# Kernel optimization log

Measured on AMD Instinct MI355X. Metric: run time of the kernel, lower is better.

Reference implementation:

```python
import jax, jax.numpy as jnp
import numpy as np

B, T, L, H, D = 1024, 128, 16, 512, 64

def setup_inputs() -> dict:
    key = jax.random.key(0)
    ks = jax.random.split(key, 12)
    s = 0.05  # param init scale to keep gates in a sane range
    return {
        "labels": jax.random.normal(ks[0], (B, L), jnp.float32),
        "z": jax.random.normal(ks[1], (T, B, H), jnp.float32),
        "W1": s * jax.random.normal(ks[2], (H, L), jnp.float32),
        "b1": jnp.zeros((H,), jnp.float32),
        "W2": s * jax.random.normal(ks[3], (H, H), jnp.float32),
        "b2": jnp.zeros((H,), jnp.float32),
        "W3": s * jax.random.normal(ks[4], (H, H), jnp.float32),
        "Wih": s * jax.random.normal(ks[5], (4 * H, H), jnp.float32),
        "Whh": s * jax.random.normal(ks[6], (4 * H, H), jnp.float32),
        "bih": jnp.zeros((4 * H,), jnp.float32),
        "bhh": jnp.zeros((4 * H,), jnp.float32),
        "P1": s * jax.random.normal(ks[7], (H, H), jnp.float32),
        "pb1": jnp.zeros((H,), jnp.float32),
        "P2": s * jax.random.normal(ks[8], (H, H), jnp.float32),
        "pb2": jnp.zeros((H,), jnp.float32),
        "P3": s * jax.random.normal(ks[9], (D, H), jnp.float32),
        "pb3": jnp.zeros((D,), jnp.float32),
    }

def reference(labels, z, W1, b1, W2, b2, W3, Wih, Whh, bih, bhh,
              P1, pb1, P2, pb2, P3, pb3):
    # label_linear MLP: Linear-ReLU-Linear-ReLU-Linear(no bias)
    x = jax.nn.relu(labels @ W1.T + b1)
    x = jax.nn.relu(x @ W2.T + b2)
    conds = x @ W3.T                      # [B, H]

    def step(carry, zt):
        h, c = carry
        inp = conds + zt                  # noise injected each timestep
        gates = inp @ Wih.T + bih + h @ Whh.T + bhh   # [B, 4H]
        i, f, g, o = jnp.split(gates, 4, axis=-1)     # torch LSTMCell gate order
        i = jax.nn.sigmoid(i)
        f = jax.nn.sigmoid(f)
        g = jnp.tanh(g)
        o = jax.nn.sigmoid(o)
        c = f * c + i * g
        h = o * jnp.tanh(c)
        # proj MLP per step
        y = jax.nn.relu(h @ P1.T + pb1)
        y = jax.nn.relu(y @ P2.T + pb2)
        y = y @ P3.T + pb3                # [B, D]
        return (h, c), y

    h0 = jnp.zeros_like(conds)
    c0 = jnp.zeros_like(conds)
    _, ys = jax.lax.scan(step, (h0, c0), z)  # ys: [T, B, D]
    return jnp.transpose(ys, (1, 0, 2))      # [B, T, D] == torch.stack(dim=1)
```

## Files before the change

### kernel.cpp

```cpp
#include <hip/hip_runtime.h>
#include <cstdint>
#include <cstddef>

namespace {

constexpr int Bb = 1024;
constexpr int Tt = 128;
constexpr int Ll = 16;
constexpr int Hh = 512;
constexpr int Dd = 64;
constexpr int Gg = 2048;
constexpr int CH = 16;

typedef _Float16 half8 __attribute__((ext_vector_type(8)));
typedef float f32x4 __attribute__((ext_vector_type(4)));

__device__ __forceinline__ float sigm(float x) { return 1.f / (1.f + __expf(-x)); }
__device__ __forceinline__ float tanh_f(float x) { return 2.f / (1.f + __expf(-2.f * x)) - 1.f; }

__device__ __forceinline__ void gload16(const void* g, void* l) {
  __builtin_amdgcn_global_load_lds(
      (const __attribute__((address_space(1))) void*)g,
      (__attribute__((address_space(3))) void*)l, 16, 0, 0);
}

__global__ void k_wcat(const float* __restrict__ Wih, const float* __restrict__ Whh,
                       _Float16* __restrict__ Wcat) {
  int idx = blockIdx.x * 256 + threadIdx.x;
  int n = idx >> 10, k = idx & 1023;
  float v = (k < Hh) ? Wih[n * Hh + k] : Whh[n * Hh + (k - Hh)];
  Wcat[idx] = (_Float16)v;
}

__global__ void k_cvt(const float* __restrict__ src, _Float16* __restrict__ dst, int n) {
  int idx = blockIdx.x * 256 + threadIdx.x;
  if (idx < n) dst[idx] = (_Float16)src[idx];
}

__global__ void k_gbias(const float* __restrict__ a, const float* __restrict__ b,
                        float* __restrict__ o) {
  int i = blockIdx.x * 256 + threadIdx.x;
  if (i < Gg) o[i] = a[i] + b[i];
}

__global__ void k_label1(const float* __restrict__ labels, const float* __restrict__ W1,
                         const float* __restrict__ b1, _Float16* __restrict__ x1) {
  int idx = blockIdx.x * 256 + threadIdx.x;
  int b = idx >> 9, n = idx & 511;
  const float* lab = labels + b * Ll;
  const float* w = W1 + n * Ll;
  float s = b1[n];
#pragma unroll
  for (int l = 0; l < Ll; ++l) s += lab[l] * w[l];
  x1[idx] = (_Float16)fmaxf(s, 0.f);
}

__global__ void k_init(float* __restrict__ c, _Float16* __restrict__ A0,
                       const float* __restrict__ conds, const float* __restrict__ z0) {
  int idx = blockIdx.x * 256 + threadIdx.x;
  int b = idx >> 9, h = idx & 511;
  c[idx] = 0.f;
  A0[(size_t)b * 1024 + 512 + h] = (_Float16)0.f;
  A0[(size_t)b * 1024 + h] = (_Float16)(conds[idx] + z0[idx]);
}

template <int BM, int BN>
__global__ __launch_bounds__(256) void gemm_tn(
    const _Float16* __restrict__ A, int lda,
    const _Float16* __restrict__ W, int ldb,
    const float* __restrict__ bias,
    float* __restrict__ Cf, _Float16* __restrict__ Ch, int ldc,
    int K, int relu, int out_mode, int t0) {
  constexpr int BK = 64;
  __shared__ __align__(16) _Float16 lA[BM * BK];
  __shared__ __align__(16) _Float16 lB[BN * BK];
  constexpr int WM = BM / 2, WN = BN / 2;
  constexpr int MF = WM / 16, NF = WN / 16;
  const int tid = threadIdx.x;
  const int lane = tid & 63;
  const int wid = tid >> 6;
  const int wm = wid >> 1, wn = wid & 1;
  const long bm0 = (long)blockIdx.x * BM, bn0 = (long)blockIdx.y * BN;
  const int srow = tid >> 3, schunk = tid & 7;

  f32x4 zero4 = {0.f, 0.f, 0.f, 0.f};
  f32x4 acc[MF][NF];
#pragma unroll
  for (int i = 0; i < MF; ++i)
#pragma unroll
    for (int j = 0; j < NF; ++j) acc[i][j] = zero4;

  for (int k0 = 0; k0 < K; k0 += BK) {
#pragma unroll
    for (int i = 0; i < BM / 32; ++i) {
      int row = i * 32 + srow;
      int gc = schunk ^ (row & 7);
      gload16(A + (bm0 + row) * lda + k0 + gc * 8, &lA[row * BK + schunk * 8]);
    }
#pragma unroll
    for (int i = 0; i < BN / 32; ++i) {
      int row = i * 32 + srow;
      int gc = schunk ^ (row & 7);
      gload16(W + (bn0 + row) * ldb + k0 + gc * 8, &lB[row * BK + schunk * 8]);
    }
    __syncthreads();
#pragma unroll
    for (int kk = 0; kk < BK; kk += 32) {
      half8 af[MF], bf[NF];
#pragma unroll
      for (int mi = 0; mi < MF; ++mi) {
        int r = wm * WM + mi * 16 + (lane & 15);
        int c = (kk >> 3) + (lane >> 4);
        af[mi] = *(const half8*)&lA[r * BK + ((c ^ (r & 7)) << 3)];
      }
#pragma unroll
      for (int ni = 0; ni < NF; ++ni) {
        int r = wn * WN + ni * 16 + (lane & 15);
        int c = (kk >> 3) + (lane >> 4);
        bf[ni] = *(const half8*)&lB[r * BK + ((c ^ (r & 7)) << 3)];
      }
#pragma unroll
      for (int mi = 0; mi < MF; ++mi)
#pragma unroll
        for (int ni = 0; ni < NF; ++ni)
          acc[mi][ni] = __builtin_amdgcn_mfma_f32_16x16x32_f16(af[mi], bf[ni], acc[mi][ni], 0, 0, 0);
    }
    __syncthreads();
  }

#pragma unroll
  for (int mi = 0; mi < MF; ++mi) {
#pragma unroll
    for (int ni = 0; ni < NF; ++ni) {
      long col = bn0 + wn * WN + ni * 16 + (lane & 15);
      float bv = bias ? bias[col] : 0.f;
#pragma unroll
      for (int j = 0; j < 4; ++j) {
        long grow = bm0 + wm * WM + mi * 16 + (lane >> 4) * 4 + j;
        float v = acc[mi][ni][j] + bv;
        if (relu) v = fmaxf(v, 0.f);
        if (Ch) {
          Ch[grow * ldc + col] = (_Float16)v;
        } else {
          long off = out_mode ? (((grow & 1023) * Tt + t0 + (grow >> 10)) * Dd + col)
                              : (grow * ldc + col);
          Cf[off] = v;
        }
      }
    }
  }
}

__global__ __launch_bounds__(256) void step_fused(
    const _Float16* __restrict__ Acur,
    const _Float16* __restrict__ Wcat,
    const float* __restrict__ gbias,
    float* __restrict__ c,
    _Float16* __restrict__ Anext,
    _Float16* __restrict__ hchunk,
    const float* __restrict__ conds,
    const float* __restrict__ znext,
    int tloc) {
  constexpr int BK = 64;
  __shared__ __align__(16) _Float16 lA[64 * BK];
  __shared__ __align__(16) _Float16 lB[64 * BK];
  const int tid = threadIdx.x;
  const int lane = tid & 63;
  const int w = tid >> 6;
  const long bm0 = (long)blockIdx.x * 64;
  const int hc0 = blockIdx.y * 16;
  const int srow = tid >> 3, schunk = tid & 7;

  f32x4 zero4 = {0.f, 0.f, 0.f, 0.f};
  f32x4 acc[4];
#pragma unroll
  for (int i = 0; i < 4; ++i) acc[i] = zero4;

  for (int k0 = 0; k0 < 1024; k0 += BK) {
#pragma unroll
    for (int i = 0; i < 2; ++i) {
      int row = i * 32 + srow;
      int gc = schunk ^ (row & 7);
      gload16(Acur + (bm0 + row) * 1024 + k0 + gc * 8, &lA[row * BK + schunk * 8]);
    }
#pragma unroll
    for (int i = 0; i < 2; ++i) {
      int rb = i * 32 + srow;
      long grow = ((long)(rb >> 4) << 9) + hc0 + (rb & 15);
      int gc = schunk ^ (rb & 7);
      gload16(Wcat + grow * 1024 + k0 + gc * 8, &lB[rb * BK + schunk * 8]);
    }
    __syncthreads();
#pragma unroll
    for (int kk = 0; kk < BK; kk += 32) {
      int cch = (kk >> 3) + (lane >> 4);
      int ra = w * 16 + (lane & 15);
      half8 af = *(const half8*)&lA[ra * BK + (((cch ^ (ra & 7))) << 3)];
#pragma unroll
      for (int ni = 0; ni < 4; ++ni) {
        int rb = ni * 16 + (lane & 15);
        half8 bf = *(const half8*)&lB[rb * BK + (((cch ^ (rb & 7))) << 3)];
        acc[ni] = __builtin_amdgcn_mfma_f32_16x16x32_f16(af, bf, acc[ni], 0, 0, 0);
      }
    }
    __syncthreads();
  }

  const int h = hc0 + (lane & 15);
  const float bi = gbias[h];
  const float bf_ = gbias[h + 512];
  const float bg = gbias[h + 1024];
  const float bo = gbias[h + 1536];
#pragma unroll
  for (int j = 0; j < 4; ++j) {
    long b = bm0 + w * 16 + (lane >> 4) * 4 + j;
    long idx = b * 512 + h;
    float iv = sigm(acc[0][j] + bi);
    float fv = sigm(acc[1][j] + bf_);
    float gv = tanh_f(acc[2][j] + bg);
    float ov = sigm(acc[3][j] + bo);
    float cc = fv * c[idx] + iv * gv;
    c[idx] = cc;
    float hh = ov * tanh_f(cc);
    _Float16 hf = (_Float16)hh;
    Anext[b * 1024 + 512 + h] = hf;
    hchunk[(long)tloc * (Bb * Hh) + idx] = hf;
    if (znext) Anext[b * 1024 + h] = (_Float16)(conds[idx] + znext[idx]);
  }
}

}

extern "C" void kernel_launch(void* const* d_in, const int* in_sizes, int n_in,
                              void* d_out, int out_size, void* d_ws, size_t ws_size,
                              hipStream_t stream) {
  const float* labels = (const float*)d_in[0];
  const float* z      = (const float*)d_in[1];
  const float* W1     = (const float*)d_in[2];
  const float* b1     = (const float*)d_in[3];
  const float* W2     = (const float*)d_in[4];
  const float* b2     = (const float*)d_in[5];
  const float* W3     = (const float*)d_in[6];
  const float* Wih    = (const float*)d_in[7];
  const float* Whh    = (const float*)d_in[8];
  const float* bih    = (const float*)d_in[9];
  const float* bhh    = (const float*)d_in[10];
  const float* P1     = (const float*)d_in[11];
  const float* pb1    = (const float*)d_in[12];
  const float* P2     = (const float*)d_in[13];
  const float* pb2    = (const float*)d_in[14];
  const float* P3     = (const float*)d_in[15];
  const float* pb3    = (const float*)d_in[16];
  float* out = (float*)d_out;
  (void)in_sizes; (void)n_in; (void)out_size; (void)ws_size;

  char* p = (char*)d_ws;
  auto alloc = [&](size_t bytes) -> char* {
    char* r = p;
    p += (bytes + 255) & ~(size_t)255;
    return r;
  };
  _Float16* Wcat  = (_Float16*)alloc((size_t)Gg * 1024 * 2);
  _Float16* P1h   = (_Float16*)alloc((size_t)Hh * Hh * 2);
  _Float16* P2h   = (_Float16*)alloc((size_t)Hh * Hh * 2);
  _Float16* P3h   = (_Float16*)alloc((size_t)Dd * Hh * 2);
  _Float16* W2h   = (_Float16*)alloc((size_t)Hh * Hh * 2);
  _Float16* W3h   = (_Float16*)alloc((size_t)Hh * Hh * 2);
  float*    gb    = (float*)alloc((size_t)Gg * 4);
  _Float16* x1    = (_Float16*)alloc((size_t)Bb * Hh * 2);
  _Float16* x2    = (_Float16*)alloc((size_t)Bb * Hh * 2);
  float*    conds = (float*)alloc((size_t)Bb * Hh * 4);
  float*    cbuf  = (float*)alloc((size_t)Bb * Hh * 4);
  _Float16* A0    = (_Float16*)alloc((size_t)Bb * 1024 * 2);
  _Float16* A1    = (_Float16*)alloc((size_t)Bb * 1024 * 2);
  _Float16* hch   = (_Float16*)alloc((size_t)CH * Bb * Hh * 2);
  _Float16* Y1    = (_Float16*)alloc((size_t)CH * Bb * Hh * 2);
  _Float16* Y2    = (_Float16*)alloc((size_t)CH * Bb * Hh * 2);

  dim3 blk(256);

  k_wcat<<<(Gg * 1024) / 256, blk, 0, stream>>>(Wih, Whh, Wcat);
  k_cvt<<<(Hh * Hh) / 256, blk, 0, stream>>>(P1, P1h, Hh * Hh);
  k_cvt<<<(Hh * Hh) / 256, blk, 0, stream>>>(P2, P2h, Hh * Hh);
  k_cvt<<<(Dd * Hh) / 256, blk, 0, stream>>>(P3, P3h, Dd * Hh);
  k_cvt<<<(Hh * Hh) / 256, blk, 0, stream>>>(W2, W2h, Hh * Hh);
  k_cvt<<<(Hh * Hh) / 256, blk, 0, stream>>>(W3, W3h, Hh * Hh);
  k_gbias<<<Gg / 256, blk, 0, stream>>>(bih, bhh, gb);

  k_label1<<<(Bb * Hh) / 256, blk, 0, stream>>>(labels, W1, b1, x1);
  gemm_tn<64, 64><<<dim3(Bb / 64, Hh / 64), blk, 0, stream>>>(
      x1, Hh, W2h, Hh, b2, nullptr, x2, Hh, Hh, 1, 0, 0);
  gemm_tn<64, 64><<<dim3(Bb / 64, Hh / 64), blk, 0, stream>>>(
      x2, Hh, W3h, Hh, nullptr, conds, nullptr, Hh, Hh, 0, 0, 0);

  k_init<<<(Bb * Hh) / 256, blk, 0, stream>>>(cbuf, A0, conds, z);

  for (int t = 0; t < Tt; ++t) {
    const _Float16* Acur = (t & 1) ? A1 : A0;
    _Float16* Anext = (t & 1) ? A0 : A1;
    const float* znext = (t + 1 < Tt) ? (z + (size_t)(t + 1) * Bb * Hh) : nullptr;
    step_fused<<<dim3(Bb / 64, Hh / 16), blk, 0, stream>>>(
        Acur, Wcat, gb, cbuf, Anext, hch, conds, znext, t & (CH - 1));
    if ((t & (CH - 1)) == (CH - 1)) {
      int t0 = t - (CH - 1);
      gemm_tn<128, 128><<<dim3(CH * Bb / 128, Hh / 128), blk, 0, stream>>>(
          hch, Hh, P1h, Hh, pb1, nullptr, Y1, Hh, Hh, 1, 0, 0);
      gemm_tn<128, 128><<<dim3(CH * Bb / 128, Hh / 128), blk, 0, stream>>>(
          Y1, Hh, P2h, Hh, pb2, nullptr, Y2, Hh, Hh, 1, 0, 0);
      gemm_tn<64, 64><<<dim3(CH * Bb / 64, Dd / 64), blk, 0, stream>>>(
          Y2, Hh, P3h, Hh, pb3, out, nullptr, Dd, Hh, 0, 1, t0);
    }
  }
}
```

Before: 2.769 ms.

## Double-buffer LDS in GEMMs, remap step blocks per XCD, enlarge chunk size

Adds double-buffered LDS staging to the generic GEMM and the fused LSTM step so the next K tile loads while MFMAs run on the current one. Remaps step_fused block indices so that blocks landing on the same XCD share weight column slices, for better L2 reuse of Wcat. Doubles the projection chunk size to 32 timesteps and merges the weight conversion kernels into one launch. Doubling LDS use may lower occupancy, and the larger chunk needs bigger scratch buffers.

After: 3.044 ms. 1.1x slower.

```diff
diff --git a/kernel.cpp b/kernel.cpp
--- a/kernel.cpp
+++ b/kernel.cpp
@@ -10,7 +10,7 @@
 constexpr int Hh = 512;
 constexpr int Dd = 64;
 constexpr int Gg = 2048;
-constexpr int CH = 16;
+constexpr int CH = 32;
 
 typedef _Float16 half8 __attribute__((ext_vector_type(8)));
 typedef float f32x4 __attribute__((ext_vector_type(4)));
@@ -32,15 +32,24 @@
   Wcat[idx] = (_Float16)v;
 }
 
-__global__ void k_cvt(const float* __restrict__ src, _Float16* __restrict__ dst, int n) {
+__global__ void k_cvt_all(const float* __restrict__ W2, const float* __restrict__ W3,
+                          const float* __restrict__ P1, const float* __restrict__ P2,
+                          const float* __restrict__ P3,
+                          const float* __restrict__ bih, const float* __restrict__ bhh,
+                          _Float16* __restrict__ W2h, _Float16* __restrict__ W3h,
+                          _Float16* __restrict__ P1h, _Float16* __restrict__ P2h,
+                          _Float16* __restrict__ P3h, float* __restrict__ gb) {
   int idx = blockIdx.x * 256 + threadIdx.x;
-  if (idx < n) dst[idx] = (_Float16)src[idx];
-}
-
-__global__ void k_gbias(const float* __restrict__ a, const float* __restrict__ b,
-                        float* __restrict__ o) {
-  int i = blockIdx.x * 256 + threadIdx.x;
-  if (i < Gg) o[i] = a[i] + b[i];
+  constexpr int Q = Hh * Hh;
+  if (idx < Q) W2h[idx] = (_Float16)W2[idx];
+  else if (idx < 2 * Q) W3h[idx - Q] = (_Float16)W3[idx - Q];
+  else if (idx < 3 * Q) P1h[idx - 2 * Q] = (_Float16)P1[idx - 2 * Q];
+  else if (idx < 4 * Q) P2h[idx - 3 * Q] = (_Float16)P2[idx - 3 * Q];
+  else if (idx < 4 * Q + Dd * Hh) P3h[idx - 4 * Q] = (_Float16)P3[idx - 4 * Q];
+  else if (idx < 4 * Q + Dd * Hh + Gg) {
+    int i = idx - 4 * Q - Dd * Hh;
+    gb[i] = bih[i] + bhh[i];
+  }
 }
 
 __global__ void k_label1(const float* __restrict__ labels, const float* __restrict__ W1,
@@ -72,8 +81,8 @@
     float* __restrict__ Cf, _Float16* __restrict__ Ch, int ldc,
     int K, int relu, int out_mode, int t0) {
   constexpr int BK = 64;
-  __shared__ __align__(16) _Float16 lA[BM * BK];
-  __shared__ __align__(16) _Float16 lB[BN * BK];
+  __shared__ __align__(16) _Float16 lA[2][BM * BK];
+  __shared__ __align__(16) _Float16 lB[2][BN * BK];
   constexpr int WM = BM / 2, WN = BN / 2;
   constexpr int MF = WM / 16, NF = WN / 16;
   const int tid = threadIdx.x;
@@ -90,20 +99,27 @@
 #pragma unroll
     for (int j = 0; j < NF; ++j) acc[i][j] = zero4;
 
-  for (int k0 = 0; k0 < K; k0 += BK) {
+  auto stage = [&](int buf, int k0) {
 #pragma unroll
     for (int i = 0; i < BM / 32; ++i) {
       int row = i * 32 + srow;
       int gc = schunk ^ (row & 7);
-      gload16(A + (bm0 + row) * lda + k0 + gc * 8, &lA[row * BK + schunk * 8]);
+      gload16(A + (bm0 + row) * lda + k0 + gc * 8, &lA[buf][row * BK + schunk * 8]);
     }
 #pragma unroll
     for (int i = 0; i < BN / 32; ++i) {
       int row = i * 32 + srow;
       int gc = schunk ^ (row & 7);
-      gload16(W + (bn0 + row) * ldb + k0 + gc * 8, &lB[row * BK + schunk * 8]);
-    }
-    __syncthreads();
+      gload16(W + (bn0 + row) * ldb + k0 + gc * 8, &lB[buf][row * BK + schunk * 8]);
+    }
+  };
+
+  const int nk = K / BK;
+  stage(0, 0);
+  __syncthreads();
+  for (int ki = 0; ki < nk; ++ki) {
+    const int cur = ki & 1;
+    if (ki + 1 < nk) stage(cur ^ 1, (ki + 1) * BK);
 #pragma unroll
     for (int kk = 0; kk < BK; kk += 32) {
       half8 af[MF], bf[NF];
@@ -111,13 +127,13 @@
       for (int mi = 0; mi < MF; ++mi) {
         int r = wm * WM + mi * 16 + (lane & 15);
         int c = (kk >> 3) + (lane >> 4);
-        af[mi] = *(const half8*)&lA[r * BK + ((c ^ (r & 7)) << 3)];
+        af[mi] = *(const half8*)&lA[cur][r * BK + ((c ^ (r & 7)) << 3)];
       }
 #pragma unroll
       for (int ni = 0; ni < NF; ++ni) {
         int r = wn * WN + ni * 16 + (lane & 15);
         int c = (kk >> 3) + (lane >> 4);
-        bf[ni] = *(const half8*)&lB[r * BK + ((c ^ (r & 7)) << 3)];
+        bf[ni] = *(const half8*)&lB[cur][r * BK + ((c ^ (r & 7)) << 3)];
       }
 #pragma unroll
       for (int mi = 0; mi < MF; ++mi)
@@ -162,13 +178,15 @@
     const float* __restrict__ znext,
     int tloc) {
   constexpr int BK = 64;
-  __shared__ __align__(16) _Float16 lA[64 * BK];
-  __shared__ __align__(16) _Float16 lB[64 * BK];
+  __shared__ __align__(16) _Float16 lA[2][64 * BK];
+  __shared__ __align__(16) _Float16 lB[2][64 * BK];
   const int tid = threadIdx.x;
   const int lane = tid & 63;
   const int w = tid >> 6;
-  const long bm0 = (long)blockIdx.x * 64;
-  const int hc0 = blockIdx.y * 16;
+  const int lin = blockIdx.x + blockIdx.y * gridDim.x;
+  const int wg = (lin & 7) * 64 + (lin >> 3);
+  const long bm0 = (long)(wg & 15) * 64;
+  const int hc0 = (wg >> 4) * 16;
   const int srow = tid >> 3, schunk = tid & 7;
 
   f32x4 zero4 = {0.f, 0.f, 0.f, 0.f};
@@ -176,30 +194,36 @@
 #pragma unroll
   for (int i = 0; i < 4; ++i) acc[i] = zero4;
 
-  for (int k0 = 0; k0 < 1024; k0 += BK) {
+  auto stage = [&](int buf, int k0) {
 #pragma unroll
     for (int i = 0; i < 2; ++i) {
       int row = i * 32 + srow;
       int gc = schunk ^ (row & 7);
-      gload16(Acur + (bm0 + row) * 1024 + k0 + gc * 8, &lA[row * BK + schunk * 8]);
+      gload16(Acur + (bm0 + row) * 1024 + k0 + gc * 8, &lA[buf][row * BK + schunk * 8]);
     }
 #pragma unroll
     for (int i = 0; i < 2; ++i) {
       int rb = i * 32 + srow;
       long grow = ((long)(rb >> 4) << 9) + hc0 + (rb & 15);
       int gc = schunk ^ (rb & 7);
-      gload16(Wcat + grow * 1024 + k0 + gc * 8, &lB[rb * BK + schunk * 8]);
-    }
-    __syncthreads();
+      gload16(Wcat + grow * 1024 + k0 + gc * 8, &lB[buf][rb * BK + schunk * 8]);
+    }
+  };
+
+  stage(0, 0);
+  __syncthreads();
+  for (int ki = 0; ki < 16; ++ki) {
+    const int cur = ki & 1;
+    if (ki < 15) stage(cur ^ 1, (ki + 1) * BK);
 #pragma unroll
     for (int kk = 0; kk < BK; kk += 32) {
       int cch = (kk >> 3) + (lane >> 4);
       int ra = w * 16 + (lane & 15);
-      half8 af = *(const half8*)&lA[ra * BK + (((cch ^ (ra & 7))) << 3)];
+      half8 af = *(const half8*)&lA[cur][ra * BK + ((cch ^ (ra & 7)) << 3)];
 #pragma unroll
       for (int ni = 0; ni < 4; ++ni) {
         int rb = ni * 16 + (lane & 15);
-        half8 bf = *(const half8*)&lB[rb * BK + (((cch ^ (rb & 7))) << 3)];
+        half8 bf = *(const half8*)&lB[cur][rb * BK + ((cch ^ (rb & 7)) << 3)];
         acc[ni] = __builtin_amdgcn_mfma_f32_16x16x32_f16(af, bf, acc[ni], 0, 0, 0);
       }
     }
@@ -280,12 +304,11 @@
   dim3 blk(256);
 
   k_wcat<<<(Gg * 1024) / 256, blk, 0, stream>>>(Wih, Whh, Wcat);
-  k_cvt<<<(Hh * Hh) / 256, blk, 0, stream>>>(P1, P1h, Hh * Hh);
-  k_cvt<<<(Hh * Hh) / 256, blk, 0, stream>>>(P2, P2h, Hh * Hh);
-  k_cvt<<<(Dd * Hh) / 256, blk, 0, stream>>>(P3, P3h, Dd * Hh);
-  k_cvt<<<(Hh * Hh) / 256, blk, 0, stream>>>(W2, W2h, Hh * Hh);
-  k_cvt<<<(Hh * Hh) / 256, blk, 0, stream>>>(W3, W3h, Hh * Hh);
-  k_gbias<<<Gg / 256, blk, 0, stream>>>(bih, bhh, gb);
+  {
+    int total = 4 * Hh * Hh + Dd * Hh + Gg;
+    k_cvt_all<<<(total + 255) / 256, blk, 0, stream>>>(
+        W2, W3, P1, P2, P3, bih, bhh, W2h, W3h, P1h, P2h, P3h, gb);
+  }
 
   k_label1<<<(Bb * Hh) / 256, blk, 0, stream>>>(labels, W1, b1, x1);
   gemm_tn<64, 64><<<dim3(Bb / 64, Hh / 64), blk, 0, stream>>>(
@@ -299,7 +322,7 @@
     const _Float16* Acur = (t & 1) ? A1 : A0;
     _Float16* Anext = (t & 1) ? A0 : A1;
     const float* znext = (t + 1 < Tt) ? (z + (size_t)(t + 1) * Bb * Hh) : nullptr;
-    step_fused<<<dim3(Bb / 64, Hh / 16), blk, 0, stream>>>(
+    step_fused<<<dim3(16, 32), blk, 0, stream>>>(
         Acur, Wcat, gb, cbuf, Anext, hch, conds, znext, t & (CH - 1));
     if ((t & (CH - 1)) == (CH - 1)) {
       int t0 = t - (CH - 1);
```
